# Kernel tuning notes

Hardware: AMD Instinct MI355X
Metric: run time of the kernel (lower is better)

Reference implementation:

```python
import jax, jax.numpy as jnp
import numpy as np

N_NODES = 100000
N_EDGES = 1600000
IN_CH, HID_CH, OUT_CH, NCLASS = 128, 256, 256, 40


def gcn_conv(x, edge_index, edge_weight, W, b):
    """PyG GCNConv: h = D^{-1/2} (A + I) D^{-1/2} (x @ W) + b, weighted edges."""
    n = x.shape[0]
    row, col = edge_index[0], edge_index[1]
    loop = jnp.arange(n)
    row = jnp.concatenate([row, loop])
    col = jnp.concatenate([col, loop])
    ew = jnp.concatenate([edge_weight, jnp.ones((n,), x.dtype)])  # self-loop weight 1
    deg = jax.ops.segment_sum(ew, col, num_segments=n)
    dinv = jnp.where(deg > 0, jax.lax.rsqrt(deg), 0.0)
    norm = dinv[row] * ew * dinv[col]            # [E+N]
    h = x @ W                                    # transform before propagate (as PyG)
    msg = h[row] * norm[:, None]                 # gather + scale, [E+N, F]
    out = jax.ops.segment_sum(msg, col, num_segments=n)  # scatter-add
    return out + b


def setup_inputs() -> dict:
    key = jax.random.key(0)
    ks = jax.random.split(key, 9)
    x = jax.random.normal(ks[0], (N_NODES, IN_CH), dtype=jnp.float32)
    edge_index = jax.random.randint(ks[1], (2, N_EDGES), 0, N_NODES, dtype=jnp.int64)
    edge_attr = jax.random.uniform(ks[2], (N_EDGES,), dtype=jnp.float32)
    s1 = 1.0 / np.sqrt(IN_CH)
    s2 = 1.0 / np.sqrt(HID_CH)
    s3 = 1.0 / np.sqrt(OUT_CH)
    W1 = jax.random.uniform(ks[3], (IN_CH, HID_CH), jnp.float32, -s1, s1)
    b1 = jnp.zeros((HID_CH,), jnp.float32)
    W2 = jax.random.uniform(ks[4], (HID_CH, OUT_CH), jnp.float32, -s2, s2)
    b2 = jnp.zeros((OUT_CH,), jnp.float32)
    fcW = jax.random.uniform(ks[5], (OUT_CH, NCLASS), jnp.float32, -s3, s3)
    fcb = jax.random.uniform(ks[6], (NCLASS,), jnp.float32, -s3, s3)
    return {"x": x, "edge_index": edge_index, "edge_attr": edge_attr,
            "W1": W1, "b1": b1, "W2": W2, "b2": b2, "fcW": fcW, "fcb": fcb}


def reference(x, edge_index, edge_attr, W1, b1, W2, b2, fcW, fcb):
    # eval mode: dropout is identity
    h = jax.nn.relu(gcn_conv(x, edge_index, edge_attr, W1, b1))
    h = jax.nn.relu(gcn_conv(h, edge_index, edge_attr, W2, b2))
    return h @ fcW + fcb
```

## Files before the change

kernel.cpp:

```cpp
#include <hip/hip_runtime.h>

#define NODES 100000
#define EDGES 1600000

typedef __attribute__((ext_vector_type(4))) float floatx4;
typedef _Float16 h16;
typedef __attribute__((ext_vector_type(4))) _Float16 h16x4;
typedef __attribute__((ext_vector_type(8))) _Float16 h16x8;
typedef __attribute__((ext_vector_type(8))) _Float16 half8;

#define WSCALE 64.0f
#define WINV   (1.0f / 64.0f)

__device__ inline void load_lds16(void* lds, const void* g) {
    __builtin_amdgcn_global_load_lds((const __attribute__((address_space(1))) void*)g,
                                     (__attribute__((address_space(3))) void*)lds, 16, 0, 0);
}

__device__ inline float meta_w(unsigned m) {
    return (float)__builtin_bit_cast(h16, (unsigned short)(m & 0x7FFFu));
}

__global__ __launch_bounds__(256) void k_init(unsigned long long* __restrict__ packed, int n) {
    int i = blockIdx.x * 256 + threadIdx.x;
    if (i < n) packed[i] = 0ull;
}

__device__ inline void w_split(const float* W, h16* Wh, h16* Wl, int idx, int K) {
    int k = idx >> 8, nn = idx & 255;
    float v = W[idx] * WSCALE;
    h16 h = (h16)v;
    h16 l = (h16)(v - (float)h);
    Wh[nn * K + k] = h;
    Wl[nn * K + k] = l;
}

__global__ __launch_bounds__(256) void k_hist(unsigned long long* __restrict__ packed,
                                              unsigned short* __restrict__ rank,
                                              const int* __restrict__ col,
                                              const float* __restrict__ ew, int e,
                                              const float* __restrict__ W1, h16* __restrict__ W1h, h16* __restrict__ W1l,
                                              const float* __restrict__ W2, h16* __restrict__ W2h, h16* __restrict__ W2l,
                                              const float* __restrict__ x, h16* __restrict__ x16, int n) {
    int b = blockIdx.x;
    if (b < 6250) {
        int i = b * 256 + threadIdx.x;
        if (i < e) {
            int c = col[i];
            unsigned long long v = (1ull << 40) |
                (unsigned long long)__float2uint_rn(ew[i] * 1048576.0f);
            unsigned long long old = atomicAdd(&packed[c], v);
            rank[i] = (unsigned short)(old >> 40);
        }
    } else if (b < 6378) {
        w_split(W1, W1h, W1l, (b - 6250) * 256 + threadIdx.x, 128);
    } else if (b < 6634) {
        w_split(W2, W2h, W2l, (b - 6378) * 256 + threadIdx.x, 256);
    } else {
        int i = (b - 6634) * 256 + threadIdx.x;
        if (i < n * 32) {
            float4 v = reinterpret_cast<const float4*>(x)[i];
            h16x4 h;
            h.x = (h16)v.x; h.y = (h16)v.y; h.z = (h16)v.z; h.w = (h16)v.w;
            reinterpret_cast<h16x4*>(x16)[i] = h;
        }
    }
}

__global__ __launch_bounds__(256) void k_scan1(const unsigned long long* __restrict__ packed,
                                               int* __restrict__ rowptr,
                                               int* __restrict__ partials,
                                               float* __restrict__ dinv, int n) {
    __shared__ int wtot[4];
    const int tid = threadIdx.x, lane = tid & 63, wid = tid >> 6;
    int i = blockIdx.x * 256 + tid;
    int v = 0;
    if (i < n) {
        unsigned long long p = packed[i];
        v = (int)(p >> 40);
        float deg = 1.0f + (float)(p & 0xFFFFFFFFFFull) * (1.0f / 1048576.0f);
        dinv[i] = rsqrtf(deg);
    }
    int incl = v;
#pragma unroll
    for (int off = 1; off < 64; off <<= 1) {
        int t = __shfl_up(incl, off, 64);
        if (lane >= off) incl += t;
    }
    if (lane == 63) wtot[wid] = incl;
    __syncthreads();
    int woff = 0;
    for (int k = 0; k < wid; ++k) woff += wtot[k];
    if (i < n) rowptr[i] = woff + incl - v;
    if (tid == 255) partials[blockIdx.x] = woff + incl;
}

__global__ __launch_bounds__(256) void k_scan3(int* __restrict__ rowptr,
                                               const int* __restrict__ partials, int n) {
    __shared__ int wsum[4];
    const int tid = threadIdx.x, lane = tid & 63, wid = tid >> 6;
    const int b = blockIdx.x;
    int v = 0;
    for (int t = tid; t < b; t += 256) v += partials[t];
#pragma unroll
    for (int off = 32; off > 0; off >>= 1) v += __shfl_down(v, off, 64);
    if (lane == 0) wsum[wid] = v;
    __syncthreads();
    int base = wsum[0] + wsum[1] + wsum[2] + wsum[3];
    int i = b * 256 + tid;
    if (i < n) rowptr[i] += base;
    if (b == 0 && tid == 0) rowptr[n] = EDGES;
}

__global__ __launch_bounds__(256) void k_build(const int* __restrict__ rowptr,
                                               const unsigned short* __restrict__ rank,
                                               unsigned* __restrict__ meta,
                                               const int* __restrict__ row, const int* __restrict__ col,
                                               const float* __restrict__ ew,
                                               const float* __restrict__ dinv, int e) {
    int i = blockIdx.x * 256 + threadIdx.x;
    if (i >= e) return;
    int r = row[i], c = col[i];
    float w = dinv[r] * ew[i] * dinv[c];
    unsigned short wb = __builtin_bit_cast(unsigned short, (h16)w);
    meta[rowptr[c] + rank[i]] = ((unsigned)r << 15) | wb;
}

__global__ __launch_bounds__(256) void k_gather_x(h16* __restrict__ Xa,
                                                  const h16* __restrict__ x16,
                                                  const float* __restrict__ dinv,
                                                  const int* __restrict__ rowptr,
                                                  const unsigned* __restrict__ meta, int n) {
    int node = (blockIdx.x << 2) + (threadIdx.x >> 6);
    if (node >= n) return;
    const int lane = threadIdx.x & 63;
    const int half = lane >> 5;
    const int cb = (lane & 31) << 2;
    float a0[4] = {}, a1[4] = {};
    int p = rowptr[node];
    const int end = rowptr[node + 1];
    for (; p + 3 < end; p += 4) {
        unsigned m0 = meta[p + half], m1 = meta[p + half + 2];
        h16x4 h0 = *(const h16x4*)(x16 + (size_t)(m0 >> 15) * 128 + cb);
        h16x4 h1 = *(const h16x4*)(x16 + (size_t)(m1 >> 15) * 128 + cb);
        float w0 = meta_w(m0), w1 = meta_w(m1);
#pragma unroll
        for (int j = 0; j < 4; ++j) {
            a0[j] = fmaf((float)h0[j], w0, a0[j]);
            a1[j] = fmaf((float)h1[j], w1, a1[j]);
        }
    }
    for (; p + 1 < end; p += 2) {
        unsigned m0 = meta[p + half];
        h16x4 h0 = *(const h16x4*)(x16 + (size_t)(m0 >> 15) * 128 + cb);
        float w0 = meta_w(m0);
#pragma unroll
        for (int j = 0; j < 4; ++j) a0[j] = fmaf((float)h0[j], w0, a0[j]);
    }
    if (half == 0 && p < end) {
        unsigned m0 = meta[p];
        h16x4 h0 = *(const h16x4*)(x16 + (size_t)(m0 >> 15) * 128 + cb);
        float w0 = meta_w(m0);
#pragma unroll
        for (int j = 0; j < 4; ++j) a1[j] = fmaf((float)h0[j], w0, a1[j]);
    }
#pragma unroll
    for (int j = 0; j < 4; ++j) a0[j] += a1[j];
#pragma unroll
    for (int j = 0; j < 4; ++j) a0[j] += __shfl(a0[j], lane + 32);
    if (half == 0) {
        float s = dinv[node]; s = s * s;
        h16x4 sv = *(const h16x4*)(x16 + (size_t)node * 128 + cb);
        h16x4 o;
#pragma unroll
        for (int j = 0; j < 4; ++j) o[j] = (h16)fmaf((float)sv[j], s, a0[j]);
        __builtin_nontemporal_store(o, (h16x4*)(Xa + (size_t)node * 128 + cb));
    }
}

__global__ __launch_bounds__(256) void k_gather_y(h16* __restrict__ Y,
                                                  const h16* __restrict__ P1,
                                                  const float* __restrict__ dinv,
                                                  const int* __restrict__ rowptr,
                                                  const unsigned* __restrict__ meta, int n) {
    int node = (blockIdx.x << 2) + (threadIdx.x >> 6);
    if (node >= n) return;
    const int lane = threadIdx.x & 63;
    const int half = lane >> 5;
    const int cb = (lane & 31) << 3;
    float a0[8] = {}, a1[8] = {};
    int p = rowptr[node];
    const int end = rowptr[node + 1];
    for (; p + 3 < end; p += 4) {
        unsigned m0 = meta[p + half], m1 = meta[p + half + 2];
        h16x8 h0 = *(const h16x8*)(P1 + (size_t)(m0 >> 15) * 256 + cb);
        h16x8 h1 = *(const h16x8*)(P1 + (size_t)(m1 >> 15) * 256 + cb);
        float w0 = meta_w(m0), w1 = meta_w(m1);
#pragma unroll
        for (int j = 0; j < 8; ++j) {
            a0[j] = fmaf((float)h0[j], w0, a0[j]);
            a1[j] = fmaf((float)h1[j], w1, a1[j]);
        }
    }
    for (; p + 1 < end; p += 2) {
        unsigned m0 = meta[p + half];
        h16x8 h0 = *(const h16x8*)(P1 + (size_t)(m0 >> 15) * 256 + cb);
        float w0 = meta_w(m0);
#pragma unroll
        for (int j = 0; j < 8; ++j) a0[j] = fmaf((float)h0[j], w0, a0[j]);
    }
    if (half == 0 && p < end) {
        unsigned m0 = meta[p];
        h16x8 h0 = *(const h16x8*)(P1 + (size_t)(m0 >> 15) * 256 + cb);
        float w0 = meta_w(m0);
#pragma unroll
        for (int j = 0; j < 8; ++j) a1[j] = fmaf((float)h0[j], w0, a1[j]);
    }
#pragma unroll
    for (int j = 0; j < 8; ++j) a0[j] += a1[j];
#pragma unroll
    for (int j = 0; j < 8; ++j) a0[j] += __shfl(a0[j], lane + 32);
    if (half == 0) {
        float s = dinv[node]; s = s * s;
        h16x8 sv = *(const h16x8*)(P1 + (size_t)node * 256 + cb);
        h16x8 o;
#pragma unroll
        for (int j = 0; j < 8; ++j) o[j] = (h16)fmaf((float)sv[j], s, a0[j]);
        __builtin_nontemporal_store(o, (h16x8*)(Y + (size_t)node * 256 + cb));
    }
}

template<bool NT>
__global__ __launch_bounds__(256) void k_gemm(const h16* __restrict__ Ag,
                                              const h16* __restrict__ Bhg,
                                              const h16* __restrict__ Blg,
                                              h16* __restrict__ Out,
                                              const float* __restrict__ bias,
                                              int M, int K) {
    __shared__ __attribute__((aligned(16))) char ldsA[8192];
    __shared__ __attribute__((aligned(16))) char ldsBh[8192];
    __shared__ __attribute__((aligned(16))) char ldsBl[8192];
    const int tid = threadIdx.x;
    const int lane = tid & 63, wid = tid >> 6;
    const int quad = lane >> 4, l16 = lane & 15;
    const int rowBase = blockIdx.x * 128;
    const int colBase = blockIdx.y * 128;
    const int wm = (wid & 1) * 64, wn = (wid >> 1) * 64;

    floatx4 acc[4][4] = {};

    const int c0 = wid * 64 + lane;
    const int c1 = c0 + 256;
    const int r0 = ((c0 >> 6) << 4) + (c0 & 15), q0 = (c0 >> 4) & 3;
    const int r1 = ((c1 >> 6) << 4) + (c1 & 15), q1 = (c1 >> 4) & 3;
    const size_t aoff0 = (size_t)(rowBase + r0) * K + q0 * 8;
    const size_t aoff1 = (size_t)(rowBase + r1) * K + q1 * 8;
    const size_t boff0 = (size_t)(colBase + r0) * K + q0 * 8;
    const size_t boff1 = (size_t)(colBase + r1) * K + q1 * 8;
    const int lo0 = (wid * 64) * 16;
    const int lo1 = (256 + wid * 64) * 16;

    for (int k0 = 0; k0 < K; k0 += 32) {
        load_lds16(ldsA + lo0, Ag + aoff0 + k0);
        load_lds16(ldsA + lo1, Ag + aoff1 + k0);
        load_lds16(ldsBh + lo0, Bhg + boff0 + k0);
        load_lds16(ldsBh + lo1, Bhg + boff1 + k0);
        load_lds16(ldsBl + lo0, Blg + boff0 + k0);
        load_lds16(ldsBl + lo1, Blg + boff1 + k0);
        __syncthreads();

        const half8* vA  = (const half8*)ldsA;
        const half8* vBh = (const half8*)ldsBh;
        const half8* vBl = (const half8*)ldsBl;
        half8 af[4], bfh[4], bfl[4];
#pragma unroll
        for (int mi = 0; mi < 4; ++mi)
            af[mi] = vA[((wm >> 4) + mi) * 64 + quad * 16 + l16];
#pragma unroll
        for (int ni = 0; ni < 4; ++ni) {
            int idx = ((wn >> 4) + ni) * 64 + quad * 16 + l16;
            bfh[ni] = vBh[idx];
            bfl[ni] = vBl[idx];
        }
#pragma unroll
        for (int mi = 0; mi < 4; ++mi)
#pragma unroll
            for (int ni = 0; ni < 4; ++ni) {
                acc[mi][ni] = __builtin_amdgcn_mfma_f32_16x16x32_f16(af[mi], bfh[ni], acc[mi][ni], 0, 0, 0);
                acc[mi][ni] = __builtin_amdgcn_mfma_f32_16x16x32_f16(af[mi], bfl[ni], acc[mi][ni], 0, 0, 0);
            }
        __syncthreads();
    }

#pragma unroll
    for (int mi = 0; mi < 4; ++mi) {
#pragma unroll
        for (int r = 0; r < 4; ++r) {
            int grow = rowBase + wm + mi * 16 + quad * 4 + r;
            if (grow < M) {
#pragma unroll
                for (int ni = 0; ni < 4; ++ni) {
                    int gcol = colBase + wn + ni * 16 + l16;
                    float v = fmaxf(acc[mi][ni][r] * WINV + bias[gcol], 0.f);
                    if (NT) __builtin_nontemporal_store((h16)v, Out + (size_t)grow * 256 + gcol);
                    else Out[(size_t)grow * 256 + gcol] = (h16)v;
                }
            }
        }
    }
}

__global__ __launch_bounds__(256) void k_fc(float* __restrict__ out, const h16* __restrict__ X,
                                            const float* __restrict__ W, const float* __restrict__ bias,
                                            int M) {
    __shared__ __attribute__((aligned(16))) char ldsB[24576];
    __shared__ __attribute__((aligned(16))) char ldsA[8192];
    const int tid = threadIdx.x;
    const int lane = tid & 63, wid = tid >> 6;
    const int quad = lane >> 4, l16 = lane & 15;
    const int rowBase = blockIdx.x * 128;

    for (int c = tid; c < 1536; c += 256) {
        int idx = c & 63, s = (c >> 6) & 7, t = c >> 9;
        int q = idx >> 4, nn = t * 16 + (idx & 15);
        int kb = s * 32 + q * 8;
        h16x8 v = {};
        if (nn < 40) {
#pragma unroll
            for (int j = 0; j < 8; ++j) v[j] = (h16)W[(kb + j) * 40 + nn];
        }
        *reinterpret_cast<h16x8*>(ldsB + c * 16) = v;
    }

    floatx4 acc[2][3] = {};
    const int c0 = wid * 64 + lane;
    const int c1 = c0 + 256;
    const int r0 = ((c0 >> 6) << 4) + (c0 & 15), q0 = (c0 >> 4) & 3;
    const int r1 = ((c1 >> 6) << 4) + (c1 & 15), q1 = (c1 >> 4) & 3;

    for (int s = 0; s < 8; ++s) {
        int k0 = s * 32;
        load_lds16(ldsA + c0 * 16, X + (size_t)(rowBase + r0) * 256 + k0 + q0 * 8);
        load_lds16(ldsA + c1 * 16, X + (size_t)(rowBase + r1) * 256 + k0 + q1 * 8);
        __syncthreads();
        const half8* vA = (const half8*)ldsA;
        const half8* vB = (const half8*)ldsB;
        half8 af[2];
#pragma unroll
        for (int mi = 0; mi < 2; ++mi)
            af[mi] = vA[(wid * 2 + mi) * 64 + quad * 16 + l16];
#pragma unroll
        for (int t = 0; t < 3; ++t) {
            half8 bf = vB[(t * 8 + s) * 64 + quad * 16 + l16];
#pragma unroll
            for (int mi = 0; mi < 2; ++mi)
                acc[mi][t] = __builtin_amdgcn_mfma_f32_16x16x32_f16(af[mi], bf, acc[mi][t], 0, 0, 0);
        }
        __syncthreads();
    }

#pragma unroll
    for (int mi = 0; mi < 2; ++mi)
#pragma unroll
        for (int r = 0; r < 4; ++r) {
            int grow = rowBase + wid * 32 + mi * 16 + quad * 4 + r;
            if (grow < M) {
#pragma unroll
                for (int t = 0; t < 3; ++t) {
                    int gcol = t * 16 + l16;
                    if (gcol < 40)
                        out[(size_t)grow * 40 + gcol] = acc[mi][t][r] + bias[gcol];
                }
            }
        }
}

extern "C" void kernel_launch(void* const* d_in, const int* in_sizes, int n_in,
                              void* d_out, int out_size, void* d_ws, size_t ws_size,
                              hipStream_t stream) {
    const float* x   = (const float*)d_in[0];
    const int*   ei  = (const int*)d_in[1];
    const float* ea  = (const float*)d_in[2];
    const float* W1  = (const float*)d_in[3];
    const float* b1  = (const float*)d_in[4];
    const float* W2  = (const float*)d_in[5];
    const float* b2  = (const float*)d_in[6];
    const float* fcW = (const float*)d_in[7];
    const float* fcb = (const float*)d_in[8];
    float* out = (float*)d_out;

    const int n = NODES, e = EDGES;
    const int* row = ei;
    const int* col = ei + e;

    char* ws = (char*)d_ws;
    char*  Areg   = ws;
    char*  Breg   = ws + 102400000u;
    float* dinv   = (float*)(ws + 204800000u);
    unsigned long long* packed = (unsigned long long*)(ws + 205200000u);
    int*   rowptr = (int*)  (ws + 206000000u);
    unsigned* meta = (unsigned*)(ws + 206400016u);
    h16*   W1h    = (h16*)  (ws + 212800016u);
    h16*   W1l    = (h16*)  (ws + 212865552u);
    h16*   W2h    = (h16*)  (ws + 212931088u);
    h16*   W2l    = (h16*)  (ws + 213062160u);

    int* partials = (int*)Areg;
    h16* Xa16 = (h16*)Areg;
    h16* x16  = (h16*)(Areg + 25600000u);
    h16* Yh   = (h16*)Areg;
    unsigned short* rank = (unsigned short*)Breg;
    h16* P1   = (h16*)Breg;
    h16* P2h  = (h16*)(Breg + 51200000u);

    const int nb = (n + 255) / 256;
    const int eb = e / 256;

    k_init<<<nb, 256, 0, stream>>>(packed, n);
    k_hist<<<19134, 256, 0, stream>>>(packed, rank, col, ea, e,
                                      W1, W1h, W1l, W2, W2h, W2l, x, x16, n);
    k_scan1<<<nb, 256, 0, stream>>>(packed, rowptr, partials, dinv, n);
    k_scan3<<<nb, 256, 0, stream>>>(rowptr, partials, n);
    k_build<<<eb, 256, 0, stream>>>(rowptr, rank, meta, row, col, ea, dinv, e);

    dim3 gg((n + 127) / 128, 2);

    k_gather_x<<<(n + 3) / 4, 256, 0, stream>>>(Xa16, x16, dinv, rowptr, meta, n);
    k_gemm<false><<<gg, 256, 0, stream>>>(Xa16, W1h, W1l, P1, b1, n, 128);

    k_gather_y<<<(n + 3) / 4, 256, 0, stream>>>(Yh, P1, dinv, rowptr, meta, n);
    k_gemm<true><<<gg, 256, 0, stream>>>(Yh, W2h, W2l, P2h, b2, n, 256);

    k_fc<<<(n + 127) / 128, 256, 0, stream>>>(out, P2h, fcW, fcb, n);
}
```

Measured before the change: 556.0 us.

## Widen GEMM tile to full 256 columns, shrink degree atomics to 32-bit

The GEMM now computes all 256 output columns per block, using a 128x256 tile and doubled B LDS buffers. The A tile is loaded once rather than once per column half, and launch bounds request two blocks per CU. The degree/count histogram is packed into 32-bit atomics (7-bit count, 25-bit fixed-point weight) instead of 64-bit, with nontemporal edge loads and a memset replacing the init kernel. Risks include higher register pressure from the 4x8 accumulators, and the narrower packing can overflow if a node's in-degree reaches 128 or its weight sum grows large.

```diff
diff --git a/kernel.cpp b/kernel.cpp
--- a/kernel.cpp
+++ b/kernel.cpp
@@ -19,11 +19,6 @@
 
 __device__ inline float meta_w(unsigned m) {
     return (float)__builtin_bit_cast(h16, (unsigned short)(m & 0x7FFFu));
-}
-
-__global__ __launch_bounds__(256) void k_init(unsigned long long* __restrict__ packed, int n) {
-    int i = blockIdx.x * 256 + threadIdx.x;
-    if (i < n) packed[i] = 0ull;
 }
 
 __device__ inline void w_split(const float* W, h16* Wh, h16* Wl, int idx, int K) {
@@ -35,7 +30,7 @@
     Wl[nn * K + k] = l;
 }
 
-__global__ __launch_bounds__(256) void k_hist(unsigned long long* __restrict__ packed,
+__global__ __launch_bounds__(256) void k_hist(unsigned* __restrict__ packed,
                                               unsigned short* __restrict__ rank,
                                               const int* __restrict__ col,
                                               const float* __restrict__ ew, int e,
@@ -46,11 +41,11 @@
     if (b < 6250) {
         int i = b * 256 + threadIdx.x;
         if (i < e) {
-            int c = col[i];
-            unsigned long long v = (1ull << 40) |
-                (unsigned long long)__float2uint_rn(ew[i] * 1048576.0f);
-            unsigned long long old = atomicAdd(&packed[c], v);
-            rank[i] = (unsigned short)(old >> 40);
+            int c = __builtin_nontemporal_load(col + i);
+            float w = __builtin_nontemporal_load(ew + i);
+            unsigned v = (1u << 25) | __float2uint_rn(w * 262144.0f);
+            unsigned old = atomicAdd(&packed[c], v);
+            rank[i] = (unsigned short)(old >> 25);
         }
     } else if (b < 6378) {
         w_split(W1, W1h, W1l, (b - 6250) * 256 + threadIdx.x, 128);
@@ -67,7 +62,7 @@
     }
 }
 
-__global__ __launch_bounds__(256) void k_scan1(const unsigned long long* __restrict__ packed,
+__global__ __launch_bounds__(256) void k_scan1(const unsigned* __restrict__ packed,
                                                int* __restrict__ rowptr,
                                                int* __restrict__ partials,
                                                float* __restrict__ dinv, int n) {
@@ -76,9 +71,9 @@
     int i = blockIdx.x * 256 + tid;
     int v = 0;
     if (i < n) {
-        unsigned long long p = packed[i];
-        v = (int)(p >> 40);
-        float deg = 1.0f + (float)(p & 0xFFFFFFFFFFull) * (1.0f / 1048576.0f);
+        unsigned p = packed[i];
+        v = (int)(p >> 25);
+        float deg = 1.0f + (float)(p & 0x1FFFFFFu) * (1.0f / 262144.0f);
         dinv[i] = rsqrtf(deg);
     }
     int incl = v;
@@ -120,8 +115,10 @@
                                                const float* __restrict__ dinv, int e) {
     int i = blockIdx.x * 256 + threadIdx.x;
     if (i >= e) return;
-    int r = row[i], c = col[i];
-    float w = dinv[r] * ew[i] * dinv[c];
+    int r = __builtin_nontemporal_load(row + i);
+    int c = __builtin_nontemporal_load(col + i);
+    float w0 = __builtin_nontemporal_load(ew + i);
+    float w = dinv[r] * w0 * dinv[c];
     unsigned short wb = __builtin_bit_cast(unsigned short, (h16)w);
     meta[rowptr[c] + rank[i]] = ((unsigned)r << 15) | wb;
 }
@@ -231,64 +228,62 @@
 }
 
 template<bool NT>
-__global__ __launch_bounds__(256) void k_gemm(const h16* __restrict__ Ag,
-                                              const h16* __restrict__ Bhg,
-                                              const h16* __restrict__ Blg,
-                                              h16* __restrict__ Out,
-                                              const float* __restrict__ bias,
-                                              int M, int K) {
+__global__ __launch_bounds__(256, 2) void k_gemm(const h16* __restrict__ Ag,
+                                                 const h16* __restrict__ Bhg,
+                                                 const h16* __restrict__ Blg,
+                                                 h16* __restrict__ Out,
+                                                 const float* __restrict__ bias,
+                                                 int M, int K) {
     __shared__ __attribute__((aligned(16))) char ldsA[8192];
-    __shared__ __attribute__((aligned(16))) char ldsBh[8192];
-    __shared__ __attribute__((aligned(16))) char ldsBl[8192];
+    __shared__ __attribute__((aligned(16))) char ldsBh[16384];
+    __shared__ __attribute__((aligned(16))) char ldsBl[16384];
     const int tid = threadIdx.x;
     const int lane = tid & 63, wid = tid >> 6;
     const int quad = lane >> 4, l16 = lane & 15;
     const int rowBase = blockIdx.x * 128;
-    const int colBase = blockIdx.y * 128;
-    const int wm = (wid & 1) * 64, wn = (wid >> 1) * 64;
-
-    floatx4 acc[4][4] = {};
-
-    const int c0 = wid * 64 + lane;
-    const int c1 = c0 + 256;
-    const int r0 = ((c0 >> 6) << 4) + (c0 & 15), q0 = (c0 >> 4) & 3;
-    const int r1 = ((c1 >> 6) << 4) + (c1 & 15), q1 = (c1 >> 4) & 3;
-    const size_t aoff0 = (size_t)(rowBase + r0) * K + q0 * 8;
-    const size_t aoff1 = (size_t)(rowBase + r1) * K + q1 * 8;
-    const size_t boff0 = (size_t)(colBase + r0) * K + q0 * 8;
-    const size_t boff1 = (size_t)(colBase + r1) * K + q1 * 8;
-    const int lo0 = (wid * 64) * 16;
-    const int lo1 = (256 + wid * 64) * 16;
+    const int wm = (wid & 1) * 64, wn = (wid >> 1) * 128;
+
+    floatx4 acc[4][8] = {};
+
+    const int cA0 = wid * 64 + lane;
+    const int cA1 = cA0 + 256;
+    const int rA0 = ((cA0 >> 6) << 4) + (cA0 & 15), qA0 = (cA0 >> 4) & 3;
+    const int rA1 = ((cA1 >> 6) << 4) + (cA1 & 15), qA1 = (cA1 >> 4) & 3;
+    const size_t aoff0 = (size_t)(rowBase + rA0) * K + qA0 * 8;
+    const size_t aoff1 = (size_t)(rowBase + rA1) * K + qA1 * 8;
 
     for (int k0 = 0; k0 < K; k0 += 32) {
-        load_lds16(ldsA + lo0, Ag + aoff0 + k0);
-        load_lds16(ldsA + lo1, Ag + aoff1 + k0);
-        load_lds16(ldsBh + lo0, Bhg + boff0 + k0);
-        load_lds16(ldsBh + lo1, Bhg + boff1 + k0);
-        load_lds16(ldsBl + lo0, Blg + boff0 + k0);
-        load_lds16(ldsBl + lo1, Blg + boff1 + k0);
+        load_lds16(ldsA + cA0 * 16, Ag + aoff0 + k0);
+        load_lds16(ldsA + cA1 * 16, Ag + aoff1 + k0);
+#pragma unroll
+        for (int i = 0; i < 4; ++i) {
+            int c = tid + i * 256;
+            int r = ((c >> 6) << 4) + (c & 15);
+            int q = (c >> 4) & 3;
+            size_t go = (size_t)r * K + k0 + q * 8;
+            load_lds16(ldsBh + c * 16, Bhg + go);
+            load_lds16(ldsBl + c * 16, Blg + go);
+        }
         __syncthreads();
 
         const half8* vA  = (const half8*)ldsA;
         const half8* vBh = (const half8*)ldsBh;
         const half8* vBl = (const half8*)ldsBl;
-        half8 af[4], bfh[4], bfl[4];
+        half8 af[4];
 #pragma unroll
         for (int mi = 0; mi < 4; ++mi)
             af[mi] = vA[((wm >> 4) + mi) * 64 + quad * 16 + l16];
 #pragma unroll
-        for (int ni = 0; ni < 4; ++ni) {
+        for (int ni = 0; ni < 8; ++ni) {
             int idx = ((wn >> 4) + ni) * 64 + quad * 16 + l16;
-            bfh[ni] = vBh[idx];
-            bfl[ni] = vBl[idx];
-        }
-#pragma unroll
-        for (int mi = 0; mi < 4; ++mi)
-#pragma unroll
-            for (int ni = 0; ni < 4; ++ni) {
-                acc[mi][ni] = __builtin_amdgcn_mfma_f32_16x16x32_f16(af[mi], bfh[ni], acc[mi][ni], 0, 0, 0);
-                acc[mi][ni] = __builtin_amdgcn_mfma_f32_16x16x32_f16(af[mi], bfl[ni], acc[mi][ni], 0, 0, 0);
+            half8 bh = vBh[idx];
+            half8 bl = vBl[idx];
+#pragma unroll
+            for (int mi = 0; mi < 4; ++mi) {
+                acc[mi][ni] = __builtin_amdgcn_mfma_f32_16x16x32_f16(af[mi], bh, acc[mi][ni], 0, 0, 0);
+                acc[mi][ni] = __builtin_amdgcn_mfma_f32_16x16x32_f16(af[mi], bl, acc[mi][ni], 0, 0, 0);
             }
+        }
         __syncthreads();
     }
 
@@ -299,8 +294,8 @@
             int grow = rowBase + wm + mi * 16 + quad * 4 + r;
             if (grow < M) {
 #pragma unroll
-                for (int ni = 0; ni < 4; ++ni) {
-                    int gcol = colBase + wn + ni * 16 + l16;
+                for (int ni = 0; ni < 8; ++ni) {
+                    int gcol = wn + ni * 16 + l16;
                     float v = fmaxf(acc[mi][ni][r] * WINV + bias[gcol], 0.f);
                     if (NT) __builtin_nontemporal_store((h16)v, Out + (size_t)grow * 256 + gcol);
                     else Out[(size_t)grow * 256 + gcol] = (h16)v;
@@ -397,13 +392,13 @@
     char*  Areg   = ws;
     char*  Breg   = ws + 102400000u;
     float* dinv   = (float*)(ws + 204800000u);
-    unsigned long long* packed = (unsigned long long*)(ws + 205200000u);
-    int*   rowptr = (int*)  (ws + 206000000u);
-    unsigned* meta = (unsigned*)(ws + 206400016u);
-    h16*   W1h    = (h16*)  (ws + 212800016u);
-    h16*   W1l    = (h16*)  (ws + 212865552u);
-    h16*   W2h    = (h16*)  (ws + 212931088u);
-    h16*   W2l    = (h16*)  (ws + 213062160u);
+    unsigned* packed = (unsigned*)(ws + 205200000u);
+    int*   rowptr = (int*)  (ws + 205600000u);
+    unsigned* meta = (unsigned*)(ws + 206000016u);
+    h16*   W1h    = (h16*)  (ws + 212400016u);
+    h16*   W1l    = (h16*)  (ws + 212465552u);
+    h16*   W2h    = (h16*)  (ws + 212531088u);
+    h16*   W2l    = (h16*)  (ws + 212662160u);
 
     int* partials = (int*)Areg;
     h16* Xa16 = (h16*)Areg;
@@ -416,20 +411,20 @@
     const int nb = (n + 255) / 256;
     const int eb = e / 256;
 
-    k_init<<<nb, 256, 0, stream>>>(packed, n);
+    hipMemsetAsync(packed, 0, 400000u, stream);
     k_hist<<<19134, 256, 0, stream>>>(packed, rank, col, ea, e,
                                       W1, W1h, W1l, W2, W2h, W2l, x, x16, n);
     k_scan1<<<nb, 256, 0, stream>>>(packed, rowptr, partials, dinv, n);
     k_scan3<<<nb, 256, 0, stream>>>(rowptr, partials, n);
     k_build<<<eb, 256, 0, stream>>>(rowptr, rank, meta, row, col, ea, dinv, e);
 
-    dim3 gg((n + 127) / 128, 2);
+    const int gb = (n + 127) / 128;
 
     k_gather_x<<<(n + 3) / 4, 256, 0, stream>>>(Xa16, x16, dinv, rowptr, meta, n);
-    k_gemm<false><<<gg, 256, 0, stream>>>(Xa16, W1h, W1l, P1, b1, n, 128);
+    k_gemm<false><<<gb, 256, 0, stream>>>(Xa16, W1h, W1l, P1, b1, n, 128);
 
     k_gather_y<<<(n + 3) / 4, 256, 0, stream>>>(Yh, P1, dinv, rowptr, meta, n);
-    k_gemm<true><<<gg, 256, 0, stream>>>(Yh, W2h, W2l, P2h, b2, n, 256);
+    k_gemm<true><<<gb, 256, 0, stream>>>(Yh, W2h, W2l, P2h, b2, n, 256);
 
     k_fc<<<(n + 127) / 128, 256, 0, stream>>>(out, P2h, fcW, fcb, n);
 }
```

After: 538.9 us. 3.1% less time.
